# Performance work log

Hardware: AMD Instinct MI355X
Metric: run time of the kernel (lower is better)

## Reference

```python
import jax, jax.numpy as jnp
import numpy as np

EPS_COS = 1e-8   # torch cosine_similarity eps
ATT_EPS = 1e-6   # LinearAttention eps
LN_EPS = 1e-5    # nn.LayerNorm default eps
NHEAD = 8
WS = 8           # window_size
TOPK = 16
C = 256          # embed_dim (hardcoded 256 in original gather)


def layer_norm(x, w, b):
    m = x.mean(-1, keepdims=True)
    v = ((x - m) ** 2).mean(-1, keepdims=True)
    return (x - m) / jnp.sqrt(v + LN_EPS) * w + b


def linear_attention(q, k, v):
    # q,k,v: [N, L, H, D]
    Q = jax.nn.elu(q) + 1.0
    K = jax.nn.elu(k) + 1.0
    L = v.shape[1]
    v = v / L
    KV = jnp.einsum('nshd,nshv->nhdv', K, v)
    Z = 1.0 / (jnp.einsum('nlhd,nhd->nlh', Q, K.sum(axis=1)) + ATT_EPS)
    return jnp.einsum('nlhd,nhdv,nlh->nlhv', Q, KV, Z) * L


def encoder_layer(x, source, Wq, Wk, Wv, Wm, W1, W2, n1w, n1b, n2w, n2b):
    bs, _, d = x.shape
    dim = d // NHEAD
    q = (x @ Wq).reshape(bs, -1, NHEAD, dim)
    k = (source @ Wk).reshape(bs, -1, NHEAD, dim)
    v = (source @ Wv).reshape(bs, -1, NHEAD, dim)
    msg = linear_attention(q, k, v).reshape(bs, -1, d) @ Wm
    msg = layer_norm(msg, n1w, n1b)
    msg = jax.nn.relu(jnp.concatenate([x, msg], axis=-1) @ W1) @ W2
    msg = layer_norm(msg, n2w, n2b)
    return x + msg


def topk_select(x, k):
    # x: [BN, S, C]; cosine similarity of each token to window mean, then topk
    avg = x.mean(axis=1, keepdims=True)                        # [BN,1,C]
    dot = (avg * x).sum(axis=-1)                               # [BN,S]
    na = jnp.maximum(jnp.linalg.norm(avg, axis=-1), EPS_COS)   # [BN,1]
    nb = jnp.maximum(jnp.linalg.norm(x, axis=-1), EPS_COS)     # [BN,S]
    cos = dot / (na * nb)
    _, idx = jax.lax.top_k(cos, k)                             # [BN,k]
    sel = jnp.take_along_axis(x, idx[:, :, None], axis=1)      # [BN,k,C]
    return sel, idx


def scatter_add(x, idx, src):
    # x: [BN,S,C], idx: [BN,k], src: [BN,k,C]
    BN, S, c = x.shape
    flat_idx = (jnp.arange(BN)[:, None] * S + idx).reshape(-1)
    return x.reshape(BN * S, c).at[flat_idx].add(src.reshape(-1, c)).reshape(BN, S, c)


def window_reverse_nchw(windows, ws, H, W):
    c = windows.shape[-1]
    x = windows.transpose(0, 2, 1).reshape(-1, H // ws, W // ws, c, ws, ws)
    return x.transpose(0, 3, 1, 4, 2, 5).reshape(-1, c, H, W)


def setup_inputs() -> dict:
    key = jax.random.key(0)
    ks = jax.random.split(key, 8)
    BN = 2 * 2304  # batch * nums_window
    s = 1.0 / np.sqrt(C)
    return {
        'x_win_attn': jax.random.normal(ks[0], (BN, WS * WS, C), jnp.float32),
        's_win_attn': jax.random.normal(ks[1], (BN, WS * WS, C), jnp.float32),
        'Wq': jax.random.normal(ks[2], (C, C), jnp.float32) * s,
        'Wk': jax.random.normal(ks[3], (C, C), jnp.float32) * s,
        'Wv': jax.random.normal(ks[4], (C, C), jnp.float32) * s,
        'Wmerge': jax.random.normal(ks[5], (C, C), jnp.float32) * s,
        'W1': jax.random.normal(ks[6], (2 * C, 2 * C), jnp.float32) * (1.0 / np.sqrt(2 * C)),
        'W2': jax.random.normal(ks[7], (2 * C, C), jnp.float32) * (1.0 / np.sqrt(2 * C)),
        'n1w': jnp.ones((C,), jnp.float32),
        'n1b': jnp.zeros((C,), jnp.float32),
        'n2w': jnp.ones((C,), jnp.float32),
        'n2b': jnp.zeros((C,), jnp.float32),
        'batch_size': 2,
        'nums_window': 2304,
        'h': 384,
        'w': 384,
    }


def reference(x_win_attn, s_win_attn, Wq, Wk, Wv, Wmerge, W1, W2,
              n1w, n1b, n2w, n2b, batch_size, nums_window, h, w):
    # 'cross' attention path of WinTopKAttention
    sel1, idx1 = topk_select(x_win_attn, TOPK)
    sel2, _ = topk_select(s_win_attn, TOPK)
    sel1 = sel1.reshape(batch_size, nums_window * TOPK, C)
    sel2 = sel2.reshape(batch_size, nums_window * TOPK, C)
    out = encoder_layer(sel1, sel2, Wq, Wk, Wv, Wmerge, W1, W2, n1w, n1b, n2w, n2b)
    out = out.reshape(batch_size * nums_window, TOPK, C)
    combined = scatter_add(x_win_attn, idx1, out)
    return window_reverse_nchw(combined, WS, h, w)
```

## Files before the change

### kernel.cpp

```cpp
#include <hip/hip_runtime.h>
#include <math.h>

static constexpr int BATCH = 2;
static constexpr int NWIN  = 2304;
static constexpr int BN    = BATCH * NWIN;
static constexpr int S     = 64;
static constexpr int CDIM  = 256;
static constexpr int TOPK_ = 16;
static constexpr int TROWS = BN * TOPK_;
static constexpr int LB    = NWIN * TOPK_;
static constexpr int HW    = 384;
static constexpr int KVSZ  = 8448;
static constexpr int KVBLKS_PER_BATCH = 64;

typedef unsigned short u16;
typedef __attribute__((ext_vector_type(4))) float  f32x4;
typedef __attribute__((ext_vector_type(8))) short  bf16x8;

__device__ inline u16 f2bf(float f) {
    unsigned u = __float_as_uint(f);
    return (u16)((u + 0x7fffu + ((u >> 16) & 1u)) >> 16);
}

__device__ inline void load_lds16(const void* g, void* l) {
    __builtin_amdgcn_global_load_lds(
        (const __attribute__((address_space(1))) unsigned int*)g,
        (__attribute__((address_space(3))) unsigned int*)l, 16, 0, 0);
}

__global__ __launch_bounds__(256) void wconv_k(
    const float* __restrict__ W, u16* __restrict__ Wt, int Kd, int Nd)
{
    const int t = blockIdx.x * 256 + threadIdx.x;
    if (t >= Kd * Nd) return;
    const int k = t / Nd, n = t - k * Nd;
    Wt[(size_t)n * Kd + k] = f2bf(W[t]);
}

__global__ __launch_bounds__(256) void topk_gather_k(
    const float* __restrict__ xin, const float* __restrict__ sin,
    u16* __restrict__ catp, u16* __restrict__ selS, int* __restrict__ idxX)
{
    __shared__ float  xl[64 * 257];
    __shared__ double avgd[256];
    __shared__ double cosv[64];
    __shared__ int    slots[16];

    const int w   = blockIdx.x;
    const bool isX = (blockIdx.y == 0);
    const int tid = threadIdx.x;
    const float* src = (isX ? xin : sin) + (size_t)w * S * CDIM;

    for (int t = 0; t < 64; ++t)
        xl[t * 257 + tid] = src[t * CDIM + tid];
    __syncthreads();

    double sm = 0.0;
    for (int t = 0; t < 64; ++t) sm += (double)xl[t * 257 + tid];
    avgd[tid] = sm * (1.0 / 64.0);
    __syncthreads();

    const int tok = tid >> 2, p = tid & 3;
    double sd = 0.0, sn = 0.0, sa = 0.0;
    for (int i = 0; i < 64; ++i) {
        const int c = p * 64 + i;
        const double xv = (double)xl[tok * 257 + c];
        const double av = avgd[c];
        sd += av * xv; sn += xv * xv; sa += av * av;
    }
    sd += __shfl_xor(sd, 1); sd += __shfl_xor(sd, 2);
    sn += __shfl_xor(sn, 1); sn += __shfl_xor(sn, 2);
    sa += __shfl_xor(sa, 1); sa += __shfl_xor(sa, 2);
    if (p == 0) {
        double na = sqrt(sa); if (na < 1e-8) na = 1e-8;
        double nb = sqrt(sn); if (nb < 1e-8) nb = 1e-8;
        cosv[tok] = sd / (na * nb);
    }
    __syncthreads();

    if (tid < 64) {
        const double ct = cosv[tid];
        int r = 0;
        for (int j = 0; j < 64; ++j) {
            const double cj = cosv[j];
            r += (cj > ct) || (cj == ct && j < tid);
        }
        if (r < TOPK_) slots[r] = tid;
    }
    __syncthreads();

    if (isX) {
        if (tid < TOPK_) idxX[w * TOPK_ + tid] = slots[tid];
        for (int j = 0; j < TOPK_; ++j) {
            const int t = slots[j];
            catp[((size_t)w * TOPK_ + j) * 512 + tid] = f2bf(xl[t * 257 + tid]);
        }
    } else {
        for (int j = 0; j < TOPK_; ++j) {
            const int t = slots[j];
            selS[((size_t)w * TOPK_ + j) * 256 + tid] = f2bf(xl[t * 257 + tid]);
        }
    }
}

template<int EPI, bool OUTBF>
__global__ __launch_bounds__(256) void gemm_bf16_k(
    const u16* __restrict__ A, int lda,
    const u16* __restrict__ Bt, int K,
    void* __restrict__ Cout, int ldc)
{
    __shared__ u16 As[128 * 32];
    __shared__ u16 Bs[128 * 32];

    const int m0 = blockIdx.y * 128, n0 = blockIdx.x * 128;
    const int tid = threadIdx.x;
    const int lane = tid & 63, w = tid >> 6;
    const int wr = w >> 1, wc = w & 1;

    f32x4 acc[4][4];
#pragma unroll
    for (int i = 0; i < 4; ++i)
#pragma unroll
        for (int j = 0; j < 4; ++j)
            acc[i][j] = (f32x4){0.f, 0.f, 0.f, 0.f};

    const int rsel = lane & 15, ksel = (lane >> 4) * 8;

    for (int k0 = 0; k0 < K; k0 += 32) {
#pragma unroll
        for (int i = 0; i < 2; ++i) {
            const int c = w * 2 + i;
            const int e = c * 512 + lane * 8;
            const int row = e >> 5, col = e & 31;
            load_lds16(&A[(size_t)(m0 + row) * lda + k0 + col], &As[c * 512]);
            load_lds16(&Bt[(size_t)(n0 + row) * K  + k0 + col], &Bs[c * 512]);
        }
        __syncthreads();

        bf16x8 af[4], bfr[4];
#pragma unroll
        for (int i = 0; i < 4; ++i)
            af[i] = *(const bf16x8*)&As[(wr * 64 + i * 16 + rsel) * 32 + ksel];
#pragma unroll
        for (int j = 0; j < 4; ++j)
            bfr[j] = *(const bf16x8*)&Bs[(wc * 64 + j * 16 + rsel) * 32 + ksel];
#pragma unroll
        for (int i = 0; i < 4; ++i)
#pragma unroll
            for (int j = 0; j < 4; ++j)
                acc[i][j] = __builtin_amdgcn_mfma_f32_16x16x32_bf16(
                    af[i], bfr[j], acc[i][j], 0, 0, 0);
        __syncthreads();
    }

    const int crow = (lane >> 4) * 4, ccol = lane & 15;
#pragma unroll
    for (int i = 0; i < 4; ++i) {
#pragma unroll
        for (int j = 0; j < 4; ++j) {
#pragma unroll
            for (int r = 0; r < 4; ++r) {
                float v = acc[i][j][r];
                if (EPI == 1) v = (v > 0.f) ? (v + 1.f) : __expf(v);
                if (EPI == 2) v = (v > 0.f) ? v : 0.f;
                const size_t off = (size_t)(m0 + wr * 64 + i * 16 + crow + r) * ldc
                                 + (n0 + wc * 64 + j * 16 + ccol);
                if (OUTBF) ((u16*)Cout)[off] = f2bf(v);
                else       ((float*)Cout)[off] = v;
            }
        }
    }
}

__global__ __launch_bounds__(256) void kv_part_k(
    const float* __restrict__ Kb, const float* __restrict__ Vb,
    float* __restrict__ part)
{
    __shared__ float Kt[16][256];
    __shared__ float Vt[16][256];

    const int bk = blockIdx.x;
    const int batch = bk >> 6, slot = bk & 63;
    const size_t r0 = (size_t)batch * LB + (size_t)slot * 576;
    const int h = threadIdx.x >> 5, e = threadIdx.x & 31;

    float acc[32] = {};
    float ks = 0.f;

    for (int tile = 0; tile < 36; ++tile) {
        const size_t rb = r0 + tile * 16;
        for (int i = 0; i < 16; ++i) {
            Kt[i][threadIdx.x] = Kb[(rb + i) * 256 + threadIdx.x];
            Vt[i][threadIdx.x] = Vb[(rb + i) * 256 + threadIdx.x];
        }
        __syncthreads();
        for (int s = 0; s < 16; ++s) {
            const float vv = Vt[s][(h << 5) + e];
            ks += Kt[s][(h << 5) + e];
#pragma unroll
            for (int d = 0; d < 32; ++d)
                acc[d] += Kt[s][(h << 5) + d] * vv;
        }
        __syncthreads();
    }

    float* pb = part + (size_t)bk * KVSZ;
    for (int d = 0; d < 32; ++d)
        pb[((h << 5) + d) * 32 + e] = acc[d];
    pb[8192 + threadIdx.x] = ks;
}

__global__ __launch_bounds__(256) void kv_reduce_k(
    const float* __restrict__ part, float* __restrict__ fin)
{
    const int g = blockIdx.x * 256 + threadIdx.x;
    if (g >= 2 * KVSZ) return;
    const int b = g / KVSZ, i = g - b * KVSZ;
    float s = 0.f;
    for (int p = 0; p < KVBLKS_PER_BATCH; ++p)
        s += part[(size_t)(b * KVBLKS_PER_BATCH + p) * KVSZ + i];
    fin[(size_t)b * KVSZ + i] = s;
}

__global__ __launch_bounds__(256) void attn_apply_k(
    const float* __restrict__ Q, const float* __restrict__ KV,
    u16* __restrict__ outp)
{
    __shared__ float kvs[8192];
    __shared__ float kss[256];
    __shared__ float qs[8][256];

    const int t0 = blockIdx.x * 64;
    const int batch = t0 / LB;
    const float* kvb = KV + (size_t)batch * KVSZ;
    for (int i = threadIdx.x; i < 8192; i += 256) kvs[i] = kvb[i];
    kss[threadIdx.x] = kvb[8192 + threadIdx.x];
    const int h = threadIdx.x >> 5, e = threadIdx.x & 31;
    __syncthreads();

    for (int o = 0; o < 64; o += 8) {
        __syncthreads();
        for (int i = 0; i < 8; ++i)
            qs[i][threadIdx.x] = Q[(size_t)(t0 + o + i) * 256 + threadIdx.x];
        __syncthreads();
        for (int tt = 0; tt < 8; ++tt) {
            const float* qh = &qs[tt][h << 5];
            float zq = 0.f, res = 0.f;
#pragma unroll
            for (int d = 0; d < 32; ++d) {
                const float qd = qh[d];
                zq  += qd * kss[(h << 5) + d];
                res += qd * kvs[((h << 5) + d) * 32 + e];
            }
            outp[(size_t)(t0 + o + tt) * 256 + threadIdx.x] = f2bf(res / (zq + 1e-6f));
        }
    }
}

template<bool OUTBF, bool ADDG>
__global__ __launch_bounds__(256) void ln_k(
    const float* __restrict__ in, void* __restrict__ outp, int ldo,
    const float* __restrict__ gw, const float* __restrict__ gb,
    const float* __restrict__ xsrc, const int* __restrict__ idx)
{
    const int lane = threadIdx.x & 63, wid = threadIdx.x >> 6;
    const size_t row = (size_t)blockIdx.x * 4 + wid;
    const float* ip = in + row * 256;

    float xv[4];
#pragma unroll
    for (int i = 0; i < 4; ++i) xv[i] = ip[i * 64 + lane];
    float s = xv[0] + xv[1] + xv[2] + xv[3];
#pragma unroll
    for (int m = 1; m < 64; m <<= 1) s += __shfl_xor(s, m);
    const float mean = s * (1.f / 256.f);
    float v = 0.f;
#pragma unroll
    for (int i = 0; i < 4; ++i) { const float d = xv[i] - mean; v += d * d; }
#pragma unroll
    for (int m = 1; m < 64; m <<= 1) v += __shfl_xor(v, m);
    const float rstd = rsqrtf(v * (1.f / 256.f) + 1e-5f);

    const float* xr = nullptr;
    if (ADDG) xr = xsrc + ((size_t)(row >> 4) * 64 + idx[row]) * 256;

#pragma unroll
    for (int i = 0; i < 4; ++i) {
        const int c = i * 64 + lane;
        float o = (xv[i] - mean) * rstd * gw[c] + gb[c];
        if (ADDG) o += xr[c];
        if (OUTBF) ((u16*)outp)[row * ldo + c] = f2bf(o);
        else       ((float*)outp)[row * ldo + c] = o;
    }
}

__global__ __launch_bounds__(256) void combine_reverse_k(
    const float* __restrict__ xin, const int* __restrict__ idxX,
    const float* __restrict__ outsel, float* __restrict__ outp)
{
    __shared__ float tile[128 * 33];
    __shared__ int   sidx[32];

    const int p  = blockIdx.x;
    const int c0 = blockIdx.y * 32;
    const int b  = p / 1152;
    const int rem = p % 1152;
    const int wy  = rem / 24, wxp = rem % 24;
    const int w0  = b * NWIN + wy * 48 + wxp * 2;
    const int tid = threadIdx.x;

    if (tid < 32) sidx[tid] = idxX[(w0 + (tid >> 4)) * TOPK_ + (tid & 15)];

    {
        const int r = tid >> 1, half = tid & 1;
        const int wl = r >> 6, t = r & 63;
        const float* srcp = xin + ((size_t)(w0 + wl) * 64 + t) * 256 + c0 + half * 16;
        const float4 v0 = ((const float4*)srcp)[0];
        const float4 v1 = ((const float4*)srcp)[1];
        const float4 v2 = ((const float4*)srcp)[2];
        const float4 v3 = ((const float4*)srcp)[3];
        float* dst = &tile[r * 33 + half * 16];
        dst[0] = v0.x; dst[1] = v0.y; dst[2]  = v0.z; dst[3]  = v0.w;
        dst[4] = v1.x; dst[5] = v1.y; dst[6]  = v1.z; dst[7]  = v1.w;
        dst[8] = v2.x; dst[9] = v2.y; dst[10] = v2.z; dst[11] = v2.w;
        dst[12] = v3.x; dst[13] = v3.y; dst[14] = v3.z; dst[15] = v3.w;
    }
    __syncthreads();

    for (int it = 0; it < 4; ++it) {
        const int rid = it * 8 + (tid >> 5);
        const int cc  = tid & 31;
        const int wl  = rid >> 4, j = rid & 15;
        const int t   = sidx[rid];
        tile[((wl << 6) + t) * 33 + cc] +=
            outsel[((size_t)(w0 + wl) * TOPK_ + j) * 256 + c0 + cc];
    }
    __syncthreads();

    const int chalf = tid >> 7;
    const int pix = tid & 127;
    const int dy = pix >> 4, x16 = pix & 15;
    const int wl = x16 >> 3, dx = x16 & 7;
    const int rr = (wl << 6) + dy * 8 + dx;
    const size_t obase = (((size_t)b * 256 + c0 + chalf) * HW + (wy * 8 + dy)) * HW
                       + wxp * 16 + x16;
    for (int cc = 0; cc < 32; cc += 2)
        outp[obase + (size_t)cc * (HW * HW)] = tile[rr * 33 + cc + chalf];
}

extern "C" void kernel_launch(void* const* d_in, const int* in_sizes, int n_in,
                              void* d_out, int out_size, void* d_ws, size_t ws_size,
                              hipStream_t stream)
{
    const float* x   = (const float*)d_in[0];
    const float* s   = (const float*)d_in[1];
    const float* Wq  = (const float*)d_in[2];
    const float* Wk  = (const float*)d_in[3];
    const float* Wv  = (const float*)d_in[4];
    const float* Wm  = (const float*)d_in[5];
    const float* W1  = (const float*)d_in[6];
    const float* W2  = (const float*)d_in[7];
    const float* n1w = (const float*)d_in[8];
    const float* n1b = (const float*)d_in[9];
    const float* n2w = (const float*)d_in[10];
    const float* n2b = (const float*)d_in[11];
    float* out = (float*)d_out;

    char* ws = (char*)d_ws;
    int*   idxX   = (int*)ws;
    float* KVpart = (float*)(ws + 294912);
    float* KVfin  = (float*)(ws + 4620288);
    u16*   Wqt    = (u16*)(ws + 4687872);
    u16*   Wkt    = (u16*)(ws + 4818944);
    u16*   Wvt    = (u16*)(ws + 4950016);
    u16*   Wmt    = (u16*)(ws + 5081088);
    u16*   W1t    = (u16*)(ws + 5212160);
    u16*   W2t    = (u16*)(ws + 5736448);
    float* Qf     = (float*)(ws + 5998592);
    float* Kf     = (float*)(ws + 81496064);
    float* Vf     = (float*)(ws + 156993536);

    u16* catA  = (u16*)d_out;
    u16* selSb = (u16*)((char*)d_out + 75497472);
    u16* msgA  = (u16*)((char*)d_out + 113246208);
    u16* Hb    = (u16*)((char*)d_out + 150994944);

    wconv_k<<<dim3(256),  256, 0, stream>>>(Wq, Wqt, 256, 256);
    wconv_k<<<dim3(256),  256, 0, stream>>>(Wk, Wkt, 256, 256);
    wconv_k<<<dim3(256),  256, 0, stream>>>(Wv, Wvt, 256, 256);
    wconv_k<<<dim3(256),  256, 0, stream>>>(Wm, Wmt, 256, 256);
    wconv_k<<<dim3(1024), 256, 0, stream>>>(W1, W1t, 512, 512);
    wconv_k<<<dim3(512),  256, 0, stream>>>(W2, W2t, 512, 256);

    topk_gather_k<<<dim3(BN, 2), 256, 0, stream>>>(x, s, catA, selSb, idxX);

    gemm_bf16_k<1, false><<<dim3(2, 576), 256, 0, stream>>>(catA, 512, Wqt, 256, Qf, 256);
    gemm_bf16_k<1, false><<<dim3(2, 576), 256, 0, stream>>>(selSb, 256, Wkt, 256, Kf, 256);
    gemm_bf16_k<0, false><<<dim3(2, 576), 256, 0, stream>>>(selSb, 256, Wvt, 256, Vf, 256);

    kv_part_k<<<dim3(2 * KVBLKS_PER_BATCH), 256, 0, stream>>>(Kf, Vf, KVpart);
    kv_reduce_k<<<dim3((2 * KVSZ + 255) / 256), 256, 0, stream>>>(KVpart, KVfin);

    attn_apply_k<<<dim3(TROWS / 64), 256, 0, stream>>>(Qf, KVfin, msgA);

    gemm_bf16_k<0, false><<<dim3(2, 576), 256, 0, stream>>>(msgA, 256, Wmt, 256, Kf, 256);
    ln_k<true, false><<<dim3(TROWS / 4), 256, 0, stream>>>(Kf, catA + 256, 512, n1w, n1b, nullptr, nullptr);

    gemm_bf16_k<2, true ><<<dim3(4, 576), 256, 0, stream>>>(catA, 512, W1t, 512, Hb, 512);
    gemm_bf16_k<0, false><<<dim3(2, 576), 256, 0, stream>>>(Hb, 512, W2t, 512, Qf, 256);

    ln_k<false, true><<<dim3(TROWS / 4), 256, 0, stream>>>(Qf, Kf, 256, n2w, n2b, x, idxX);

    combine_reverse_k<<<dim3(BN / 2, 8), 256, 0, stream>>>(x, idxX, Kf, out);
}
```

Baseline: 811.1 us.

## Store intermediates in bf16, merge weight conversions, double KV partial blocks

```diff
diff --git a/kernel.cpp b/kernel.cpp
--- a/kernel.cpp
+++ b/kernel.cpp
@@ -11,7 +11,8 @@
 static constexpr int LB    = NWIN * TOPK_;
 static constexpr int HW    = 384;
 static constexpr int KVSZ  = 8448;
-static constexpr int KVBLKS_PER_BATCH = 64;
+static constexpr int KVB   = 128;
+static constexpr int KVTOK = LB / KVB;
 
 typedef unsigned short u16;
 typedef __attribute__((ext_vector_type(4))) float  f32x4;
@@ -20,6 +21,9 @@
 __device__ inline u16 f2bf(float f) {
     unsigned u = __float_as_uint(f);
     return (u16)((u + 0x7fffu + ((u >> 16) & 1u)) >> 16);
+}
+__device__ inline float bf2f(u16 b) {
+    return __uint_as_float(((unsigned)b) << 16);
 }
 
 __device__ inline void load_lds16(const void* g, void* l) {
@@ -28,11 +32,22 @@
         (__attribute__((address_space(3))) unsigned int*)l, 16, 0, 0);
 }
 
-__global__ __launch_bounds__(256) void wconv_k(
-    const float* __restrict__ W, u16* __restrict__ Wt, int Kd, int Nd)
-{
-    const int t = blockIdx.x * 256 + threadIdx.x;
-    if (t >= Kd * Nd) return;
+__global__ __launch_bounds__(256) void wconv_all_k(
+    const float* __restrict__ Wq, const float* __restrict__ Wk,
+    const float* __restrict__ Wv, const float* __restrict__ Wm,
+    const float* __restrict__ W1, const float* __restrict__ W2,
+    u16* __restrict__ Wqt, u16* __restrict__ Wkt, u16* __restrict__ Wvt,
+    u16* __restrict__ Wmt, u16* __restrict__ W1t, u16* __restrict__ W2t)
+{
+    int t = blockIdx.x * 256 + threadIdx.x;
+    const float* W; u16* Wt; int Nd, Kd;
+    if (t < 262144) {
+        const int sel = t >> 16; t &= 65535;
+        W  = (sel == 0 ? Wq  : sel == 1 ? Wk  : sel == 2 ? Wv  : Wm);
+        Wt = (sel == 0 ? Wqt : sel == 1 ? Wkt : sel == 2 ? Wvt : Wmt);
+        Nd = 256; Kd = 256;
+    } else if (t < 524288) { W = W1; Wt = W1t; Nd = 512; Kd = 512; t -= 262144; }
+    else                   { W = W2; Wt = W2t; Nd = 256; Kd = 512; t -= 524288; }
     const int k = t / Nd, n = t - k * Nd;
     Wt[(size_t)n * Kd + k] = f2bf(W[t]);
 }
@@ -41,32 +56,33 @@
     const float* __restrict__ xin, const float* __restrict__ sin,
     u16* __restrict__ catp, u16* __restrict__ selS, int* __restrict__ idxX)
 {
-    __shared__ float  xl[64 * 257];
     __shared__ double avgd[256];
     __shared__ double cosv[64];
     __shared__ int    slots[16];
 
-    const int w   = blockIdx.x;
+    const int w    = blockIdx.x;
     const bool isX = (blockIdx.y == 0);
-    const int tid = threadIdx.x;
+    const int tid  = threadIdx.x;
     const float* src = (isX ? xin : sin) + (size_t)w * S * CDIM;
 
-    for (int t = 0; t < 64; ++t)
-        xl[t * 257 + tid] = src[t * CDIM + tid];
-    __syncthreads();
-
     double sm = 0.0;
-    for (int t = 0; t < 64; ++t) sm += (double)xl[t * 257 + tid];
+    for (int t = 0; t < 64; ++t) sm += (double)src[t * CDIM + tid];
     avgd[tid] = sm * (1.0 / 64.0);
     __syncthreads();
 
     const int tok = tid >> 2, p = tid & 3;
+    const float* rowp = src + tok * CDIM;
     double sd = 0.0, sn = 0.0, sa = 0.0;
-    for (int i = 0; i < 64; ++i) {
-        const int c = p * 64 + i;
-        const double xv = (double)xl[tok * 257 + c];
-        const double av = avgd[c];
-        sd += av * xv; sn += xv * xv; sa += av * av;
+    for (int ii = 0; ii < 16; ++ii) {
+        const int c = p * 64 + ii * 4;
+        const float4 xv4 = *(const float4*)&rowp[c];
+        const float xs[4] = {xv4.x, xv4.y, xv4.z, xv4.w};
+#pragma unroll
+        for (int q = 0; q < 4; ++q) {
+            const double xv = (double)xs[q];
+            const double av = avgd[c + q];
+            sd += av * xv; sn += xv * xv; sa += av * av;
+        }
     }
     sd += __shfl_xor(sd, 1); sd += __shfl_xor(sd, 2);
     sn += __shfl_xor(sn, 1); sn += __shfl_xor(sn, 2);
@@ -93,21 +109,21 @@
         if (tid < TOPK_) idxX[w * TOPK_ + tid] = slots[tid];
         for (int j = 0; j < TOPK_; ++j) {
             const int t = slots[j];
-            catp[((size_t)w * TOPK_ + j) * 512 + tid] = f2bf(xl[t * 257 + tid]);
+            catp[((size_t)w * TOPK_ + j) * 512 + tid] = f2bf(src[t * CDIM + tid]);
         }
     } else {
         for (int j = 0; j < TOPK_; ++j) {
             const int t = slots[j];
-            selS[((size_t)w * TOPK_ + j) * 256 + tid] = f2bf(xl[t * 257 + tid]);
-        }
-    }
-}
-
-template<int EPI, bool OUTBF>
+            selS[((size_t)w * TOPK_ + j) * 256 + tid] = f2bf(src[t * CDIM + tid]);
+        }
+    }
+}
+
+template<int EPI>
 __global__ __launch_bounds__(256) void gemm_bf16_k(
     const u16* __restrict__ A, int lda,
     const u16* __restrict__ Bt, int K,
-    void* __restrict__ Cout, int ldc)
+    u16* __restrict__ Cout, int ldc)
 {
     __shared__ u16 As[128 * 32];
     __shared__ u16 Bs[128 * 32];
@@ -163,35 +179,33 @@
                 float v = acc[i][j][r];
                 if (EPI == 1) v = (v > 0.f) ? (v + 1.f) : __expf(v);
                 if (EPI == 2) v = (v > 0.f) ? v : 0.f;
-                const size_t off = (size_t)(m0 + wr * 64 + i * 16 + crow + r) * ldc
-                                 + (n0 + wc * 64 + j * 16 + ccol);
-                if (OUTBF) ((u16*)Cout)[off] = f2bf(v);
-                else       ((float*)Cout)[off] = v;
+                Cout[(size_t)(m0 + wr * 64 + i * 16 + crow + r) * ldc
+                     + (n0 + wc * 64 + j * 16 + ccol)] = f2bf(v);
             }
         }
     }
 }
 
 __global__ __launch_bounds__(256) void kv_part_k(
-    const float* __restrict__ Kb, const float* __restrict__ Vb,
+    const u16* __restrict__ Kb, const u16* __restrict__ Vb,
     float* __restrict__ part)
 {
     __shared__ float Kt[16][256];
     __shared__ float Vt[16][256];
 
     const int bk = blockIdx.x;
-    const int batch = bk >> 6, slot = bk & 63;
-    const size_t r0 = (size_t)batch * LB + (size_t)slot * 576;
+    const int batch = bk >> 7, slot = bk & 127;
+    const size_t r0 = (size_t)batch * LB + (size_t)slot * KVTOK;
     const int h = threadIdx.x >> 5, e = threadIdx.x & 31;
 
     float acc[32] = {};
     float ks = 0.f;
 
-    for (int tile = 0; tile < 36; ++tile) {
+    for (int tile = 0; tile < KVTOK / 16; ++tile) {
         const size_t rb = r0 + tile * 16;
         for (int i = 0; i < 16; ++i) {
-            Kt[i][threadIdx.x] = Kb[(rb + i) * 256 + threadIdx.x];
-            Vt[i][threadIdx.x] = Vb[(rb + i) * 256 + threadIdx.x];
+            Kt[i][threadIdx.x] = bf2f(Kb[(rb + i) * 256 + threadIdx.x]);
+            Vt[i][threadIdx.x] = bf2f(Vb[(rb + i) * 256 + threadIdx.x]);
         }
         __syncthreads();
         for (int s = 0; s < 16; ++s) {
@@ -217,13 +231,13 @@
     if (g >= 2 * KVSZ) return;
     const int b = g / KVSZ, i = g - b * KVSZ;
     float s = 0.f;
-    for (int p = 0; p < KVBLKS_PER_BATCH; ++p)
-        s += part[(size_t)(b * KVBLKS_PER_BATCH + p) * KVSZ + i];
+    for (int p = 0; p < KVB; ++p)
+        s += part[(size_t)(b * KVB + p) * KVSZ + i];
     fin[(size_t)b * KVSZ + i] = s;
 }
 
 __global__ __launch_bounds__(256) void attn_apply_k(
-    const float* __restrict__ Q, const float* __restrict__ KV,
+    const u16* __restrict__ Q, const float* __restrict__ KV,
     u16* __restrict__ outp)
 {
     __shared__ float kvs[8192];
@@ -241,7 +255,7 @@
     for (int o = 0; o < 64; o += 8) {
         __syncthreads();
         for (int i = 0; i < 8; ++i)
-            qs[i][threadIdx.x] = Q[(size_t)(t0 + o + i) * 256 + threadIdx.x];
+            qs[i][threadIdx.x] = bf2f(Q[(size_t)(t0 + o + i) * 256 + threadIdx.x]);
         __syncthreads();
         for (int tt = 0; tt < 8; ++tt) {
             const float* qh = &qs[tt][h << 5];
@@ -257,19 +271,19 @@
     }
 }
 
-template<bool OUTBF, bool ADDG>
+template<bool ADDG>
 __global__ __launch_bounds__(256) void ln_k(
-    const float* __restrict__ in, void* __restrict__ outp, int ldo,
+    const u16* __restrict__ in, u16* __restrict__ outp, int ldo,
     const float* __restrict__ gw, const float* __restrict__ gb,
     const float* __restrict__ xsrc, const int* __restrict__ idx)
 {
     const int lane = threadIdx.x & 63, wid = threadIdx.x >> 6;
     const size_t row = (size_t)blockIdx.x * 4 + wid;
-    const float* ip = in + row * 256;
+    const u16* ip = in + row * 256;
 
     float xv[4];
 #pragma unroll
-    for (int i = 0; i < 4; ++i) xv[i] = ip[i * 64 + lane];
+    for (int i = 0; i < 4; ++i) xv[i] = bf2f(ip[i * 64 + lane]);
     float s = xv[0] + xv[1] + xv[2] + xv[3];
 #pragma unroll
     for (int m = 1; m < 64; m <<= 1) s += __shfl_xor(s, m);
@@ -289,14 +303,13 @@
         const int c = i * 64 + lane;
         float o = (xv[i] - mean) * rstd * gw[c] + gb[c];
         if (ADDG) o += xr[c];
-        if (OUTBF) ((u16*)outp)[row * ldo + c] = f2bf(o);
-        else       ((float*)outp)[row * ldo + c] = o;
+        outp[row * ldo + c] = f2bf(o);
     }
 }
 
 __global__ __launch_bounds__(256) void combine_reverse_k(
     const float* __restrict__ xin, const int* __restrict__ idxX,
-    const float* __restrict__ outsel, float* __restrict__ outp)
+    const u16* __restrict__ outsel, float* __restrict__ outp)
 {
     __shared__ float tile[128 * 33];
     __shared__ int   sidx[32];
@@ -333,7 +346,7 @@
         const int wl  = rid >> 4, j = rid & 15;
         const int t   = sidx[rid];
         tile[((wl << 6) + t) * 33 + cc] +=
-            outsel[((size_t)(w0 + wl) * TOPK_ + j) * 256 + c0 + cc];
+            bf2f(outsel[((size_t)(w0 + wl) * TOPK_ + j) * 256 + c0 + cc]);
     }
     __syncthreads();
 
@@ -369,47 +382,45 @@
     char* ws = (char*)d_ws;
     int*   idxX   = (int*)ws;
     float* KVpart = (float*)(ws + 294912);
-    float* KVfin  = (float*)(ws + 4620288);
-    u16*   Wqt    = (u16*)(ws + 4687872);
-    u16*   Wkt    = (u16*)(ws + 4818944);
-    u16*   Wvt    = (u16*)(ws + 4950016);
-    u16*   Wmt    = (u16*)(ws + 5081088);
-    u16*   W1t    = (u16*)(ws + 5212160);
-    u16*   W2t    = (u16*)(ws + 5736448);
-    float* Qf     = (float*)(ws + 5998592);
-    float* Kf     = (float*)(ws + 81496064);
-    float* Vf     = (float*)(ws + 156993536);
+    float* KVfin  = (float*)(ws + 8945664);
+    u16*   Wqt    = (u16*)(ws + 9013248);
+    u16*   Wkt    = (u16*)(ws + 9144320);
+    u16*   Wvt    = (u16*)(ws + 9275392);
+    u16*   Wmt    = (u16*)(ws + 9406464);
+    u16*   W1t    = (u16*)(ws + 9537536);
+    u16*   W2t    = (u16*)(ws + 10061824);
+    u16*   Qb     = (u16*)(ws + 10323968);
+    u16*   Kb     = (u16*)(ws + 48072704);
+    u16*   Vb     = (u16*)(ws + 85821440);
+    u16*   Mb     = (u16*)(ws + 123570176);
+    u16*   osel   = (u16*)(ws + 161318912);
 
     u16* catA  = (u16*)d_out;
     u16* selSb = (u16*)((char*)d_out + 75497472);
     u16* msgA  = (u16*)((char*)d_out + 113246208);
     u16* Hb    = (u16*)((char*)d_out + 150994944);
 
-    wconv_k<<<dim3(256),  256, 0, stream>>>(Wq, Wqt, 256, 256);
-    wconv_k<<<dim3(256),  256, 0, stream>>>(Wk, Wkt, 256, 256);
-    wconv_k<<<dim3(256),  256, 0, stream>>>(Wv, Wvt, 256, 256);
-    wconv_k<<<dim3(256),  256, 0, stream>>>(Wm, Wmt, 256, 256);
-    wconv_k<<<dim3(1024), 256, 0, stream>>>(W1, W1t, 512, 512);
-    wconv_k<<<dim3(512),  256, 0, stream>>>(W2, W2t, 512, 256);
+    wconv_all_k<<<dim3(2560), 256, 0, stream>>>(Wq, Wk, Wv, Wm, W1, W2,
+                                                Wqt, Wkt, Wvt, Wmt, W1t, W2t);
 
     topk_gather_k<<<dim3(BN, 2), 256, 0, stream>>>(x, s, catA, selSb, idxX);
 
-    gemm_bf16_k<1, false><<<dim3(2, 576), 256, 0, stream>>>(catA, 512, Wqt, 256, Qf, 256);
-    gemm_bf16_k<1, false><<<dim3(2, 576), 256, 0, stream>>>(selSb, 256, Wkt, 256, Kf, 256);
-    gemm_bf16_k<0, false><<<dim3(2, 576), 256, 0, stream>>>(selSb, 256, Wvt, 256, Vf, 256);
-
-    kv_part_k<<<dim3(2 * KVBLKS_PER_BATCH), 256, 0, stream>>>(Kf, Vf, KVpart);
+    gemm_bf16_k<1><<<dim3(2, 576), 256, 0, stream>>>(catA, 512, Wqt, 256, Qb, 256);
+    gemm_bf16_k<1><<<dim3(2, 576), 256, 0, stream>>>(selSb, 256, Wkt, 256, Kb, 256);
+    gemm_bf16_k<0><<<dim3(2, 576), 256, 0, stream>>>(selSb, 256, Wvt, 256, Vb, 256);
+
+    kv_part_k<<<dim3(2 * KVB), 256, 0, stream>>>(Kb, Vb, KVpart);
     kv_reduce_k<<<dim3((2 * KVSZ + 255) / 256), 256, 0, stream>>>(KVpart, KVfin);
 
-    attn_apply_k<<<dim3(TROWS / 64), 256, 0, stream>>>(Qf, KVfin, msgA);
-
-    gemm_bf16_k<0, false><<<dim3(2, 576), 256, 0, stream>>>(msgA, 256, Wmt, 256, Kf, 256);
-    ln_k<true, false><<<dim3(TROWS / 4), 256, 0, stream>>>(Kf, catA + 256, 512, n1w, n1b, nullptr, nullptr);
-
-    gemm_bf16_k<2, true ><<<dim3(4, 576), 256, 0, stream>>>(catA, 512, W1t, 512, Hb, 512);
-    gemm_bf16_k<0, false><<<dim3(2, 576), 256, 0, stream>>>(Hb, 512, W2t, 512, Qf, 256);
-
-    ln_k<false, true><<<dim3(TROWS / 4), 256, 0, stream>>>(Qf, Kf, 256, n2w, n2b, x, idxX);
-
-    combine_reverse_k<<<dim3(BN / 2, 8), 256, 0, stream>>>(x, idxX, Kf, out);
-}
+    attn_apply_k<<<dim3(TROWS / 64), 256, 0, stream>>>(Qb, KVfin, msgA);
+
+    gemm_bf16_k<0><<<dim3(2, 576), 256, 0, stream>>>(msgA, 256, Wmt, 256, Mb, 256);
+    ln_k<false><<<dim3(TROWS / 4), 256, 0, stream>>>(Mb, catA + 256, 512, n1w, n1b, nullptr, nullptr);
+
+    gemm_bf16_k<2><<<dim3(4, 576), 256, 0, stream>>>(catA, 512, W1t, 512, Hb, 512);
+    gemm_bf16_k<0><<<dim3(2, 576), 256, 0, stream>>>(Hb, 512, W2t, 512, Mb, 256);
+
+    ln_k<true><<<dim3(TROWS / 4), 256, 0, stream>>>(Mb, osel, 256, n2w, n2b, x, idxX);
+
+    combine_reverse_k<<<dim3(BN / 2, 8), 256, 0, stream>>>(x, idxX, osel, out);
+}
```

Result: faster. 749.1 us (-7.6%).
